# Kernel tuning notes

Hardware: AMD Instinct MI355X
Metric: run time of the kernel (lower is better)

The kernel has to match this reference:

```python
import jax, jax.numpy as jnp
import numpy as np

B, H, W, C = 32, 32, 32, 768
E = 4          # num_experts
TOPK = 2
HD = int(C * 0.25)  # 192, expert hidden dim


def setup_inputs() -> dict:
    key = jax.random.key(0)
    ks = jax.random.split(key, 7)
    x = jax.random.normal(ks[0], (B, H, W, C), dtype=jnp.float32)
    # router: nn.Linear(C, E), weight [E, C] init N(0, 0.02), bias zeros
    router_w = jax.random.normal(ks[1], (E, C), dtype=jnp.float32) * 0.02
    router_b = jnp.zeros((E,), dtype=jnp.float32)
    # per-expert MLP: fc1 [E, HD, C], fc2 [E, C, HD] (torch Linear weight layout)
    fc1_w = jax.random.normal(ks[2], (E, HD, C), dtype=jnp.float32) * (1.0 / np.sqrt(C))
    fc1_b = jax.random.normal(ks[3], (E, HD), dtype=jnp.float32) * 0.01
    fc2_w = jax.random.normal(ks[4], (E, C, HD), dtype=jnp.float32) * (1.0 / np.sqrt(HD))
    fc2_b = jax.random.normal(ks[5], (E, C), dtype=jnp.float32) * 0.01
    return {"x": x, "router_w": router_w, "router_b": router_b,
            "fc1_w": fc1_w, "fc1_b": fc1_b, "fc2_w": fc2_w, "fc2_b": fc2_b}


def reference(x, router_w, router_b, fc1_w, fc1_b, fc2_w, fc2_b):
    b, h, w, c = x.shape
    xt = x.reshape(b, h * w, c)                              # [B, S, C]
    # --- router: softmax + top-k + renormalize ---
    logits = jnp.einsum('bsc,ec->bse', xt, router_w) + router_b
    probs = jax.nn.softmax(logits, axis=-1)                  # [B, S, E]
    topk_w, topk_idx = jax.lax.top_k(probs, TOPK)            # [B, S, K]
    topk_w = topk_w / (jnp.sum(topk_w, axis=-1, keepdims=True) + 1e-8)
    # per-expert combine weight: sum over k of weight where idx==e -> [B, S, E]
    combine = jnp.sum(jax.nn.one_hot(topk_idx, E, dtype=xt.dtype)
                      * topk_w[..., None], axis=-2)          # [B, S, E]
    # --- all experts densely (same math as masked gather/scatter) ---
    # fc1 + exact GELU: [B, S, E, HD]
    hmid = jax.nn.gelu(jnp.einsum('bsc,ehc->bseh', xt, fc1_w) + fc1_b,
                       approximate=False)
    # weight tokens before fc2 to avoid [B,S,E,C] intermediate
    hw = hmid * combine[..., None]                           # [B, S, E, HD]
    out = jnp.einsum('bseh,ech->bsc', hw, fc2_w)
    out = out + jnp.einsum('bse,ec->bsc', combine, fc2_b)    # weighted fc2 bias
    return out.reshape(b, h, w, c)
```

## Files before the change

kernel.cpp:

```cpp
#include <hip/hip_runtime.h>
#include <hip/hip_bf16.h>
#include <math.h>

typedef __attribute__((ext_vector_type(8))) __bf16 bf16x8;
typedef __attribute__((ext_vector_type(4))) float f32x4;
typedef __attribute__((ext_vector_type(4))) unsigned short u16x4;

#define TOKENS 32768
#define CDIM   768
#define SLOTCAP 33536
#define MT_TILES 262
#define RBLOCKS 1024

__device__ __forceinline__ void async_copy16(const void* g, void* l) {
    __builtin_amdgcn_global_load_lds(
        (const __attribute__((address_space(1))) void*)g,
        (__attribute__((address_space(3))) void*)l, 16, 0, 0);
}

__device__ __forceinline__ float fast_gelu(float v) {
    float x  = v * 0.70710678118654752f;
    float ax = fabsf(x);
    float t  = __builtin_amdgcn_rcpf(1.0f + 0.3275911f * ax);
    float poly = t * (0.254829592f +
                 t * (-0.284496736f +
                 t * (1.421413741f +
                 t * (-1.453152027f +
                 t * 1.061405429f))));
    float erfv = 1.0f - poly * __expf(-x * x);
    erfv = copysignf(erfv, x);
    return 0.5f * v * (1.0f + erfv);
}

__device__ __forceinline__ int pair_lo(int p) { return p < 3 ? 0 : (p < 5 ? 1 : 2); }
__device__ __forceinline__ int pair_hi(int p) { return p < 3 ? p + 1 : (p < 5 ? p - 1 : 3); }

__device__ __forceinline__ void bucket_offs(const int* __restrict__ meta, int* offs) {
    int run = 0;
#pragma unroll
    for (int p = 0; p < 6; ++p) {
        offs[p] = run;
        run += ((meta[p] + 127) >> 7) << 7;
    }
}

__global__ __launch_bounds__(256) void prep_weights(
    const float* __restrict__ fc1w, const float* __restrict__ fc2w,
    __hip_bfloat16* __restrict__ b1, __hip_bfloat16* __restrict__ b2t,
    int* __restrict__ slots, float2* __restrict__ swt, int* __restrict__ meta)
{
    int idx = blockIdx.x * 256 + threadIdx.x;
    if (idx < 32) meta[idx] = 0;
    if (idx < SLOTCAP) { slots[idx] = -1; swt[idx] = make_float2(0.f, 0.f); }
    b1[idx] = __float2bfloat16(fc1w[idx]);
    int c = idx / 768;
    int r = idx - c * 768;
    int e = r / 192;
    int h = r - e * 192;
    b2t[idx] = __float2bfloat16(fc2w[((size_t)e * 768 + c) * 192 + h]);
}

__global__ __launch_bounds__(256) void router_convert(
    const float* __restrict__ x, const float* __restrict__ rw,
    const float* __restrict__ rb,
    __hip_bfloat16* __restrict__ xb,
    int* __restrict__ pairid, float2* __restrict__ wpair, int* __restrict__ meta)
{
    __shared__ int rc[6];
    if (threadIdx.x < 6) rc[threadIdx.x] = 0;
    __syncthreads();

    const int wave = threadIdx.x >> 6;
    const int lane = threadIdx.x & 63;
    const int wid  = blockIdx.x * 4 + wave;
    const int el   = lane * 4;

    float4 wv[4][3];
#pragma unroll
    for (int e = 0; e < 4; ++e)
#pragma unroll
        for (int t = 0; t < 3; ++t)
            wv[e][t] = *(const float4*)(rw + e * CDIM + t * 256 + el);
    float rbv[4];
#pragma unroll
    for (int e = 0; e < 4; ++e) rbv[e] = rb[e];

    for (int it = 0; it < 8; ++it) {
        const int token = wid * 8 + it;
        const float* xr = x + (size_t)token * CDIM;

        float4 v[3];
#pragma unroll
        for (int t = 0; t < 3; ++t) v[t] = *(const float4*)(xr + t * 256 + el);

        unsigned short* xrow = (unsigned short*)xb + (size_t)token * CDIM;
#pragma unroll
        for (int t = 0; t < 3; ++t) {
            alignas(8) __hip_bfloat16 hb[4];
            hb[0] = __float2bfloat16(v[t].x);
            hb[1] = __float2bfloat16(v[t].y);
            hb[2] = __float2bfloat16(v[t].z);
            hb[3] = __float2bfloat16(v[t].w);
            *(u16x4*)(xrow + t * 256 + el) = *(const u16x4*)hb;
        }

        float s[4];
#pragma unroll
        for (int e = 0; e < 4; ++e) {
            s[e] = v[0].x * wv[e][0].x + v[0].y * wv[e][0].y
                 + v[0].z * wv[e][0].z + v[0].w * wv[e][0].w
                 + v[1].x * wv[e][1].x + v[1].y * wv[e][1].y
                 + v[1].z * wv[e][1].z + v[1].w * wv[e][1].w
                 + v[2].x * wv[e][2].x + v[2].y * wv[e][2].y
                 + v[2].z * wv[e][2].z + v[2].w * wv[e][2].w;
        }
#pragma unroll
        for (int e = 0; e < 4; ++e) {
            float vv = s[e];
            vv += __shfl_xor(vv, 32); vv += __shfl_xor(vv, 16); vv += __shfl_xor(vv, 8);
            vv += __shfl_xor(vv, 4);  vv += __shfl_xor(vv, 2);  vv += __shfl_xor(vv, 1);
            s[e] = vv;
        }
        float lg[4], p[4];
#pragma unroll
        for (int e = 0; e < 4; ++e) lg[e] = s[e] + rbv[e];
        float mx = fmaxf(fmaxf(lg[0], lg[1]), fmaxf(lg[2], lg[3]));
        float ps = 0.f;
#pragma unroll
        for (int e = 0; e < 4; ++e) { p[e] = __expf(lg[e] - mx); ps += p[e]; }
#pragma unroll
        for (int e = 0; e < 4; ++e) p[e] /= ps;
        int a = 0;
#pragma unroll
        for (int e = 1; e < 4; ++e) if (p[e] > p[a]) a = e;
        int b = (a == 0) ? 1 : 0;
#pragma unroll
        for (int e = 0; e < 4; ++e) if (e != a && p[e] > p[b]) b = e;
        float wsum = p[a] + p[b] + 1e-8f;
        if (lane == 0) {
            int lo = a < b ? a : b;
            int hi = a < b ? b : a;
            int pid = (lo == 0) ? hi - 1 : (lo == 1 ? hi + 1 : 5);
            pairid[token] = pid;
            wpair[token] = make_float2(p[lo] / wsum, p[hi] / wsum);
            atomicAdd(&rc[pid], 1);
        }
    }
    __syncthreads();
    if (threadIdx.x < 6 && rc[threadIdx.x])
        atomicAdd(&meta[threadIdx.x], rc[threadIdx.x]);
}

__global__ __launch_bounds__(256) void scatter_tokens(
    const int* __restrict__ pairid, const float2* __restrict__ wpair,
    int* __restrict__ slots, float2* __restrict__ swt, int* __restrict__ meta)
{
    __shared__ int sc[6], sb[6], soff[6];
    int tid = threadIdx.x;
    if (tid < 6) sc[tid] = 0;
    __syncthreads();
    int t = blockIdx.x * 256 + tid;
    int p = pairid[t];
    int r = atomicAdd(&sc[p], 1);
    __syncthreads();
    if (tid == 0) {
        int offs[6];
        bucket_offs(meta, offs);
#pragma unroll
        for (int q = 0; q < 6; ++q) soff[q] = offs[q];
    }
    if (tid < 6) sb[tid] = sc[tid] ? atomicAdd(&meta[16 + tid], sc[tid]) : 0;
    __syncthreads();
    int pos = soff[p] + sb[p] + r;
    slots[pos] = t;
    swt[pos] = wpair[t];
}

#define BM 128
#define BN 128
#define BK 64

template <int MODE, int K, int NT>
__global__ __launch_bounds__(256) void gemm_moe(
    const __hip_bfloat16* __restrict__ A, const __hip_bfloat16* __restrict__ Bt,
    const int* __restrict__ slots, const float2* __restrict__ swt,
    const int* __restrict__ meta,
    const float* __restrict__ bias1,
    const float* __restrict__ bias2,
    __hip_bfloat16* __restrict__ HW,
    float* __restrict__ OUT)
{
    __shared__ __hip_bfloat16 smem[BM * BK * 4];

    const int tid = threadIdx.x;
    const int wave = tid >> 6, lane = tid & 63;
    const int wm = (wave >> 1) * 64, wn = (wave & 1) * 64;
    const int lrow = lane & 15, quad = lane >> 4;

    constexpr int nwg = MT_TILES * NT;
    constexpr int q = nwg >> 3, rr = nwg & 7;
    const int bid = blockIdx.x;
    const int xcd = bid & 7, sidx = bid >> 3;
    const int wg = (xcd < rr ? xcd * (q + 1) : rr * (q + 1) + (xcd - rr) * q) + sidx;
    const int by = wg / NT;
    const int bx = wg - by * NT;
    const int rowB0 = bx * BN;
    const int rowA0 = by * BM;

    int offs[6];
    bucket_offs(meta, offs);
    int pb = 0;
#pragma unroll
    for (int i = 1; i < 6; ++i) pb += (rowA0 >= offs[i]) ? 1 : 0;
    const int lo = pair_lo(pb), hi = pair_hi(pb);

    const int srow = lane >> 3;
    const int scol = ((lane & 7) ^ srow) * 8;

    size_t aoff[4], boff[4];
    __hip_bfloat16* ldsA[4];
#pragma unroll
    for (int p = 0; p < 4; ++p) {
        int c = wave * 4 + p;
        int arow = c * 8 + srow;
        if (MODE == 0) {
            int tok = slots[rowA0 + arow];
            tok = tok < 0 ? 0 : tok;
            aoff[p] = (size_t)tok * K + scol;
            int grow = rowB0 + arow;
            int gb = (grow < 192) ? lo * 192 + grow : hi * 192 + (grow - 192);
            boff[p] = (size_t)gb * K + scol;
        } else {
            aoff[p] = (size_t)(rowA0 + arow) * K + scol;
            boff[p] = (size_t)(rowB0 + arow) * 768 + scol;
        }
        ldsA[p] = smem + c * 8 * BK;
    }

    auto stage = [&](int buf, int k0) {
        int bo = buf * (2 * BM * BK);
        size_t badd = (MODE == 0) ? (size_t)k0
                    : (size_t)(k0 < 192 ? lo * 192 : hi * 192 - 192) + k0;
#pragma unroll
        for (int p = 0; p < 4; ++p) {
            async_copy16(A + aoff[p] + k0, ldsA[p] + bo);
            async_copy16(Bt + boff[p] + badd, ldsA[p] + bo + BM * BK);
        }
    };

    f32x4 acc[4][4] = {};
    constexpr int NIT = K / BK;

    stage(0, 0);
    __syncthreads();
#pragma unroll
    for (int it = 0; it < NIT; ++it) {
        if (it + 1 < NIT) stage((it + 1) & 1, (it + 1) * BK);
        const __hip_bfloat16* As = smem + (it & 1) * (2 * BM * BK);
        const __hip_bfloat16* Bs = As + BM * BK;
#pragma unroll
        for (int kk = 0; kk < BK; kk += 32) {
            bf16x8 af[4], bfr[4];
#pragma unroll
            for (int i = 0; i < 4; ++i) {
                int row = wm + i * 16 + lrow;
                int gp = ((kk >> 3) + quad) ^ (lrow & 7);
                af[i] = *(const bf16x8*)(&As[row * BK + gp * 8]);
            }
#pragma unroll
            for (int j = 0; j < 4; ++j) {
                int row = wn + j * 16 + lrow;
                int gp = ((kk >> 3) + quad) ^ (lrow & 7);
                bfr[j] = *(const bf16x8*)(&Bs[row * BK + gp * 8]);
            }
#pragma unroll
            for (int i = 0; i < 4; ++i)
#pragma unroll
                for (int j = 0; j < 4; ++j)
                    acc[i][j] = __builtin_amdgcn_mfma_f32_16x16x32_bf16(
                        af[i], bfr[j], acc[i][j], 0, 0, 0);
        }
        __syncthreads();
    }

    if (MODE == 0) {
        const bool hf = (rowB0 + wn) >= 192;
        float b1v[4];
#pragma unroll
        for (int j = 0; j < 4; ++j) {
            int col = rowB0 + wn + j * 16 + lrow;
            int ng = (col < 192) ? lo * 192 + col : hi * 192 + (col - 192);
            b1v[j] = bias1[ng];
        }
#pragma unroll
        for (int i = 0; i < 4; ++i) {
#pragma unroll
            for (int r = 0; r < 4; ++r) {
                int rowl = wm + i * 16 + quad * 4 + r;
                float2 wv = swt[rowA0 + rowl];
                float cwt = hf ? wv.y : wv.x;
                __hip_bfloat16* srow_p = &smem[rowl * BN + wn + lrow];
#pragma unroll
                for (int j = 0; j < 4; ++j) {
                    float v = fast_gelu(acc[i][j][r] + b1v[j]) * cwt;
                    srow_p[j * 16] = __float2bfloat16(v);
                }
            }
        }
        __syncthreads();
#pragma unroll
        for (int t = 0; t < 8; ++t) {
            int idx = t * 256 + tid;
            int row = idx >> 4;
            int c16 = (idx & 15) * 8;
            *(uint4*)(HW + (size_t)(rowA0 + row) * 384 + rowB0 + c16) =
                *(const uint4*)(&smem[row * BN + c16]);
        }
    } else {
        float blo[4], bhi[4];
#pragma unroll
        for (int j = 0; j < 4; ++j) {
            int col = rowB0 + wn + j * 16 + lrow;
            blo[j] = bias2[lo * 768 + col];
            bhi[j] = bias2[hi * 768 + col];
        }
        float* smf = (float*)smem;
#pragma unroll
        for (int i = 0; i < 4; ++i) {
#pragma unroll
            for (int r = 0; r < 4; ++r) {
                int rowl = wm + i * 16 + quad * 4 + r;
                float2 wv = swt[rowA0 + rowl];
                float* sr = smf + rowl * BN + wn + lrow;
#pragma unroll
                for (int j = 0; j < 4; ++j)
                    sr[j * 16] = acc[i][j][r] + wv.x * blo[j] + wv.y * bhi[j];
            }
        }
        __syncthreads();
#pragma unroll
        for (int t = 0; t < 16; ++t) {
            int idx = t * 256 + tid;
            int row = idx >> 5;
            int ch  = idx & 31;
            int tok = slots[rowA0 + row];
            if (tok >= 0)
                *(float4*)(OUT + (size_t)tok * CDIM + rowB0 + ch * 4) =
                    *(const float4*)(smf + row * BN + ch * 4);
        }
    }
}

extern "C" void kernel_launch(void* const* d_in, const int* in_sizes, int n_in,
                              void* d_out, int out_size, void* d_ws, size_t ws_size,
                              hipStream_t stream)
{
    const float* x    = (const float*)d_in[0];
    const float* rw   = (const float*)d_in[1];
    const float* rb   = (const float*)d_in[2];
    const float* fc1w = (const float*)d_in[3];
    const float* fc1b = (const float*)d_in[4];
    const float* fc2w = (const float*)d_in[5];
    const float* fc2b = (const float*)d_in[6];
    float* out = (float*)d_out;

    char* ws = (char*)d_ws;
    __hip_bfloat16* xb   = (__hip_bfloat16*)(ws);
    __hip_bfloat16* hw   = (__hip_bfloat16*)(ws + 50331648);
    __hip_bfloat16* b1   = (__hip_bfloat16*)(ws + 76087296);
    __hip_bfloat16* b2t  = (__hip_bfloat16*)(ws + 77266944);
    float2*         wpr  = (float2*)       (ws + 78446592);
    float2*         swt  = (float2*)       (ws + 78708736);
    int*            pid  = (int*)          (ws + 78977024);
    int*            slots= (int*)          (ws + 79108096);
    int*            meta = (int*)          (ws + 79242240);

    prep_weights<<<2304, 256, 0, stream>>>(fc1w, fc2w, b1, b2t, slots, swt, meta);
    router_convert<<<RBLOCKS, 256, 0, stream>>>(x, rw, rb, xb, pid, wpr, meta);
    scatter_tokens<<<TOKENS / 256, 256, 0, stream>>>(pid, wpr, slots, swt, meta);

    gemm_moe<0, 768, 3><<<MT_TILES * 3, 256, 0, stream>>>(
        xb, b1, slots, swt, meta, fc1b, nullptr, hw, nullptr);
    gemm_moe<1, 384, 6><<<MT_TILES * 6, 256, 0, stream>>>(
        hw, b2t, slots, swt, meta, nullptr, fc2b, nullptr, out);
}
```

Measured before the change: 275.8 us.

## Use full-width 128x384 tile for fc1 so gathered tokens load once

Splits the templated GEMM into dedicated fc1 and fc2 kernels. The fc1 kernel now uses 512 threads and a 128x384 output tile covering both experts' hidden units, so each block loads the gathered token rows once instead of three times across column tiles. It uses 128KB of dynamic shared memory for double-buffered A/B and for the epilogue staging. The cost is a grid of only 262 blocks with very low occupancy, which may underfill the GPU and expose memory latency.

```diff
diff --git a/kernel.cpp b/kernel.cpp
--- a/kernel.cpp
+++ b/kernel.cpp
@@ -176,18 +176,146 @@
     swt[pos] = wpair[t];
 }
 
+__global__ __launch_bounds__(512) void fc1_moe(
+    const __hip_bfloat16* __restrict__ A,
+    const __hip_bfloat16* __restrict__ Bt,
+    const int* __restrict__ slots, const float2* __restrict__ swt,
+    const int* __restrict__ meta, const float* __restrict__ bias1,
+    __hip_bfloat16* __restrict__ HW)
+{
+    extern __shared__ __hip_bfloat16 dynsm[];
+    __hip_bfloat16* Asm = dynsm;
+    __hip_bfloat16* Bsm = dynsm + 2 * 128 * 64;
+
+    const int tid = threadIdx.x;
+    const int wave = tid >> 6, lane = tid & 63;
+    const int wm = (wave >> 2) * 64;
+    const int wn = (wave & 3) * 96;
+    const int lrow = lane & 15, quad = lane >> 4;
+
+    constexpr int nwg = MT_TILES;
+    constexpr int q = nwg >> 3, rr = nwg & 7;
+    const int bid = blockIdx.x;
+    const int xcd = bid & 7, sidx = bid >> 3;
+    const int by = (xcd < rr ? xcd * (q + 1) : rr * (q + 1) + (xcd - rr) * q) + sidx;
+    const int rowA0 = by * 128;
+
+    int offs[6];
+    bucket_offs(meta, offs);
+    int pb = 0;
+#pragma unroll
+    for (int i = 1; i < 6; ++i) pb += (rowA0 >= offs[i]) ? 1 : 0;
+    const int lo = pair_lo(pb), hi = pair_hi(pb);
+
+    const int srow = lane >> 3;
+    const int scol = ((lane & 7) ^ srow) * 8;
+
+    unsigned aoff[2];
+    __hip_bfloat16* ldsA[2];
+#pragma unroll
+    for (int p = 0; p < 2; ++p) {
+        int c = wave * 2 + p;
+        int tok = slots[rowA0 + c * 8 + srow];
+        tok = tok < 0 ? 0 : tok;
+        aoff[p] = (unsigned)tok * 768u + scol;
+        ldsA[p] = Asm + c * 8 * 64;
+    }
+    unsigned boff[6];
+    __hip_bfloat16* ldsB[6];
+#pragma unroll
+    for (int p = 0; p < 6; ++p) {
+        int c = wave * 6 + p;
+        int grow = c * 8 + srow;
+        int gb = (grow < 192) ? lo * 192 + grow : hi * 192 + (grow - 192);
+        boff[p] = (unsigned)gb * 768u + scol;
+        ldsB[p] = Bsm + c * 8 * 64;
+    }
+
+    auto stage = [&](int buf, int k0) {
+#pragma unroll
+        for (int p = 0; p < 2; ++p)
+            async_copy16(A + aoff[p] + k0, ldsA[p] + buf * (128 * 64));
+#pragma unroll
+        for (int p = 0; p < 6; ++p)
+            async_copy16(Bt + boff[p] + k0, ldsB[p] + buf * (384 * 64));
+    };
+
+    f32x4 acc[4][6] = {};
+
+    stage(0, 0);
+    __syncthreads();
+#pragma unroll
+    for (int it = 0; it < 12; ++it) {
+        if (it + 1 < 12) stage((it + 1) & 1, (it + 1) * 64);
+        const __hip_bfloat16* As = Asm + (it & 1) * (128 * 64);
+        const __hip_bfloat16* Bs = Bsm + (it & 1) * (384 * 64);
+#pragma unroll
+        for (int kk = 0; kk < 64; kk += 32) {
+            bf16x8 af[4], bfr[6];
+#pragma unroll
+            for (int i = 0; i < 4; ++i) {
+                int row = wm + i * 16 + lrow;
+                int gp = ((kk >> 3) + quad) ^ (lrow & 7);
+                af[i] = *(const bf16x8*)(&As[row * 64 + gp * 8]);
+            }
+#pragma unroll
+            for (int j = 0; j < 6; ++j) {
+                int row = wn + j * 16 + lrow;
+                int gp = ((kk >> 3) + quad) ^ (lrow & 7);
+                bfr[j] = *(const bf16x8*)(&Bs[row * 64 + gp * 8]);
+            }
+#pragma unroll
+            for (int i = 0; i < 4; ++i)
+#pragma unroll
+                for (int j = 0; j < 6; ++j)
+                    acc[i][j] = __builtin_amdgcn_mfma_f32_16x16x32_bf16(
+                        af[i], bfr[j], acc[i][j], 0, 0, 0);
+        }
+        __syncthreads();
+    }
+
+    float b1v[6];
+#pragma unroll
+    for (int j = 0; j < 6; ++j) {
+        int col = wn + j * 16 + lrow;
+        int ng = (col < 192) ? lo * 192 + col : hi * 192 + (col - 192);
+        b1v[j] = bias1[ng];
+    }
+#pragma unroll
+    for (int i = 0; i < 4; ++i) {
+#pragma unroll
+        for (int r = 0; r < 4; ++r) {
+            int rowl = wm + i * 16 + quad * 4 + r;
+            float2 wv = swt[rowA0 + rowl];
+            __hip_bfloat16* sr = dynsm + rowl * 384 + wn + lrow;
+#pragma unroll
+            for (int j = 0; j < 6; ++j) {
+                float cwt = ((wn + j * 16) >= 192) ? wv.y : wv.x;
+                float v = fast_gelu(acc[i][j][r] + b1v[j]) * cwt;
+                sr[j * 16] = __float2bfloat16(v);
+            }
+        }
+    }
+    __syncthreads();
+#pragma unroll
+    for (int t = 0; t < 12; ++t) {
+        int idx = t * 512 + tid;
+        int row = idx / 48;
+        int c = idx - row * 48;
+        *(uint4*)(HW + (size_t)(rowA0 + row) * 384 + c * 8) =
+            *(const uint4*)(dynsm + row * 384 + c * 8);
+    }
+}
+
 #define BM 128
 #define BN 128
 #define BK 64
 
-template <int MODE, int K, int NT>
-__global__ __launch_bounds__(256) void gemm_moe(
-    const __hip_bfloat16* __restrict__ A, const __hip_bfloat16* __restrict__ Bt,
+__global__ __launch_bounds__(256) void fc2_moe(
+    const __hip_bfloat16* __restrict__ A,
+    const __hip_bfloat16* __restrict__ Bt,
     const int* __restrict__ slots, const float2* __restrict__ swt,
-    const int* __restrict__ meta,
-    const float* __restrict__ bias1,
-    const float* __restrict__ bias2,
-    __hip_bfloat16* __restrict__ HW,
+    const int* __restrict__ meta, const float* __restrict__ bias2,
     float* __restrict__ OUT)
 {
     __shared__ __hip_bfloat16 smem[BM * BK * 4];
@@ -197,6 +325,7 @@
     const int wm = (wave >> 1) * 64, wn = (wave & 1) * 64;
     const int lrow = lane & 15, quad = lane >> 4;
 
+    constexpr int NT = 6;
     constexpr int nwg = MT_TILES * NT;
     constexpr int q = nwg >> 3, rr = nwg & 7;
     const int bid = blockIdx.x;
@@ -223,24 +352,14 @@
     for (int p = 0; p < 4; ++p) {
         int c = wave * 4 + p;
         int arow = c * 8 + srow;
-        if (MODE == 0) {
-            int tok = slots[rowA0 + arow];
-            tok = tok < 0 ? 0 : tok;
-            aoff[p] = (size_t)tok * K + scol;
-            int grow = rowB0 + arow;
-            int gb = (grow < 192) ? lo * 192 + grow : hi * 192 + (grow - 192);
-            boff[p] = (size_t)gb * K + scol;
-        } else {
-            aoff[p] = (size_t)(rowA0 + arow) * K + scol;
-            boff[p] = (size_t)(rowB0 + arow) * 768 + scol;
-        }
+        aoff[p] = (size_t)(rowA0 + arow) * 384 + scol;
+        boff[p] = (size_t)(rowB0 + arow) * 768 + scol;
         ldsA[p] = smem + c * 8 * BK;
     }
 
     auto stage = [&](int buf, int k0) {
         int bo = buf * (2 * BM * BK);
-        size_t badd = (MODE == 0) ? (size_t)k0
-                    : (size_t)(k0 < 192 ? lo * 192 : hi * 192 - 192) + k0;
+        size_t badd = (size_t)(k0 < 192 ? lo * 192 : hi * 192 - 192) + k0;
 #pragma unroll
         for (int p = 0; p < 4; ++p) {
             async_copy16(A + aoff[p] + k0, ldsA[p] + bo);
@@ -249,7 +368,7 @@
     };
 
     f32x4 acc[4][4] = {};
-    constexpr int NIT = K / BK;
+    constexpr int NIT = 384 / BK;
 
     stage(0, 0);
     __syncthreads();
@@ -283,71 +402,36 @@
         __syncthreads();
     }
 
-    if (MODE == 0) {
-        const bool hf = (rowB0 + wn) >= 192;
-        float b1v[4];
-#pragma unroll
-        for (int j = 0; j < 4; ++j) {
-            int col = rowB0 + wn + j * 16 + lrow;
-            int ng = (col < 192) ? lo * 192 + col : hi * 192 + (col - 192);
-            b1v[j] = bias1[ng];
-        }
-#pragma unroll
-        for (int i = 0; i < 4; ++i) {
-#pragma unroll
-            for (int r = 0; r < 4; ++r) {
-                int rowl = wm + i * 16 + quad * 4 + r;
-                float2 wv = swt[rowA0 + rowl];
-                float cwt = hf ? wv.y : wv.x;
-                __hip_bfloat16* srow_p = &smem[rowl * BN + wn + lrow];
-#pragma unroll
-                for (int j = 0; j < 4; ++j) {
-                    float v = fast_gelu(acc[i][j][r] + b1v[j]) * cwt;
-                    srow_p[j * 16] = __float2bfloat16(v);
-                }
-            }
-        }
-        __syncthreads();
-#pragma unroll
-        for (int t = 0; t < 8; ++t) {
-            int idx = t * 256 + tid;
-            int row = idx >> 4;
-            int c16 = (idx & 15) * 8;
-            *(uint4*)(HW + (size_t)(rowA0 + row) * 384 + rowB0 + c16) =
-                *(const uint4*)(&smem[row * BN + c16]);
-        }
-    } else {
-        float blo[4], bhi[4];
-#pragma unroll
-        for (int j = 0; j < 4; ++j) {
-            int col = rowB0 + wn + j * 16 + lrow;
-            blo[j] = bias2[lo * 768 + col];
-            bhi[j] = bias2[hi * 768 + col];
-        }
-        float* smf = (float*)smem;
-#pragma unroll
-        for (int i = 0; i < 4; ++i) {
-#pragma unroll
-            for (int r = 0; r < 4; ++r) {
-                int rowl = wm + i * 16 + quad * 4 + r;
-                float2 wv = swt[rowA0 + rowl];
-                float* sr = smf + rowl * BN + wn + lrow;
-#pragma unroll
-                for (int j = 0; j < 4; ++j)
-                    sr[j * 16] = acc[i][j][r] + wv.x * blo[j] + wv.y * bhi[j];
-            }
-        }
-        __syncthreads();
-#pragma unroll
-        for (int t = 0; t < 16; ++t) {
-            int idx = t * 256 + tid;
-            int row = idx >> 5;
-            int ch  = idx & 31;
-            int tok = slots[rowA0 + row];
-            if (tok >= 0)
-                *(float4*)(OUT + (size_t)tok * CDIM + rowB0 + ch * 4) =
-                    *(const float4*)(smf + row * BN + ch * 4);
-        }
+    float blo[4], bhi[4];
+#pragma unroll
+    for (int j = 0; j < 4; ++j) {
+        int col = rowB0 + wn + j * 16 + lrow;
+        blo[j] = bias2[lo * 768 + col];
+        bhi[j] = bias2[hi * 768 + col];
+    }
+    float* smf = (float*)smem;
+#pragma unroll
+    for (int i = 0; i < 4; ++i) {
+#pragma unroll
+        for (int r = 0; r < 4; ++r) {
+            int rowl = wm + i * 16 + quad * 4 + r;
+            float2 wv = swt[rowA0 + rowl];
+            float* sr = smf + rowl * BN + wn + lrow;
+#pragma unroll
+            for (int j = 0; j < 4; ++j)
+                sr[j * 16] = acc[i][j][r] + wv.x * blo[j] + wv.y * bhi[j];
+        }
+    }
+    __syncthreads();
+#pragma unroll
+    for (int t = 0; t < 16; ++t) {
+        int idx = t * 256 + tid;
+        int row = idx >> 5;
+        int ch  = idx & 31;
+        int tok = slots[rowA0 + row];
+        if (tok >= 0)
+            *(float4*)(OUT + (size_t)tok * CDIM + rowB0 + ch * 4) =
+                *(const float4*)(smf + row * BN + ch * 4);
     }
 }
 
@@ -379,8 +463,8 @@
     router_convert<<<RBLOCKS, 256, 0, stream>>>(x, rw, rb, xb, pid, wpr, meta);
     scatter_tokens<<<TOKENS / 256, 256, 0, stream>>>(pid, wpr, slots, swt, meta);
 
-    gemm_moe<0, 768, 3><<<MT_TILES * 3, 256, 0, stream>>>(
-        xb, b1, slots, swt, meta, fc1b, nullptr, hw, nullptr);
-    gemm_moe<1, 384, 6><<<MT_TILES * 6, 256, 0, stream>>>(
-        hw, b2t, slots, swt, meta, nullptr, fc2b, nullptr, out);
-}
+    fc1_moe<<<MT_TILES, 512, 131072, stream>>>(
+        xb, b1, slots, swt, meta, fc1b, hw);
+    fc2_moe<<<MT_TILES * 6, 256, 0, stream>>>(
+        hw, b2t, slots, swt, meta, fc2b, out);
+}
```

New measurement: 288.9 us. 4.7% more time.

## Double K tile depth and drop LDS double buffering in MoE GEMM

Applied to the files above, without the earlier changes.

Raises the GEMM K tile from 64 to 128 and replaces the two-buffer LDS pipeline with one buffer that is loaded and then synchronised each iteration. This halves the number of K iterations and barriers, and LDS per block stays the same, so occupancy should not change. The cost is that global-to-LDS loads no longer overlap with the MFMA compute, which exposes load latency. Offsets also move to 32-bit, and the MODE 1 expert-boundary handling now works per 16-byte group because a 128-wide K tile can cross the 192 boundary.

```diff
diff --git a/kernel.cpp b/kernel.cpp
--- a/kernel.cpp
+++ b/kernel.cpp
@@ -178,7 +178,7 @@
 
 #define BM 128
 #define BN 128
-#define BK 64
+#define BK 128
 
 template <int MODE, int K, int NT>
 __global__ __launch_bounds__(256) void gemm_moe(
@@ -190,7 +190,7 @@
     __hip_bfloat16* __restrict__ HW,
     float* __restrict__ OUT)
 {
-    __shared__ __hip_bfloat16 smem[BM * BK * 4];
+    __shared__ __hip_bfloat16 smem[BM * BK + BN * BK];
 
     const int tid = threadIdx.x;
     const int wave = tid >> 6, lane = tid & 63;
@@ -214,50 +214,58 @@
     for (int i = 1; i < 6; ++i) pb += (rowA0 >= offs[i]) ? 1 : 0;
     const int lo = pair_lo(pb), hi = pair_hi(pb);
 
-    const int srow = lane >> 3;
-    const int scol = ((lane & 7) ^ srow) * 8;
-
-    size_t aoff[4], boff[4];
-    __hip_bfloat16* ldsA[4];
-#pragma unroll
-    for (int p = 0; p < 4; ++p) {
-        int c = wave * 4 + p;
-        int arow = c * 8 + srow;
+    const int sr4 = lane >> 4;
+    const int pg  = lane & 15;
+
+    unsigned aoff[8], boff[8];
+    __hip_bfloat16* ldsA[8];
+#pragma unroll
+    for (int p = 0; p < 8; ++p) {
+        int c = wave * 8 + p;
+        int rt = c * 4 + sr4;
+        int sg = pg ^ (rt & 7);
+        int sg8 = sg * 8;
         if (MODE == 0) {
-            int tok = slots[rowA0 + arow];
+            int tok = slots[rowA0 + rt];
             tok = tok < 0 ? 0 : tok;
-            aoff[p] = (size_t)tok * K + scol;
-            int grow = rowB0 + arow;
+            aoff[p] = (unsigned)tok * 768u + sg8;
+            int grow = rowB0 + rt;
             int gb = (grow < 192) ? lo * 192 + grow : hi * 192 + (grow - 192);
-            boff[p] = (size_t)gb * K + scol;
+            boff[p] = (unsigned)gb * 768u + sg8;
         } else {
-            aoff[p] = (size_t)(rowA0 + arow) * K + scol;
-            boff[p] = (size_t)(rowB0 + arow) * 768 + scol;
-        }
-        ldsA[p] = smem + c * 8 * BK;
-    }
-
-    auto stage = [&](int buf, int k0) {
-        int bo = buf * (2 * BM * BK);
-        size_t badd = (MODE == 0) ? (size_t)k0
-                    : (size_t)(k0 < 192 ? lo * 192 : hi * 192 - 192) + k0;
-#pragma unroll
-        for (int p = 0; p < 4; ++p) {
-            async_copy16(A + aoff[p] + k0, ldsA[p] + bo);
-            async_copy16(Bt + boff[p] + badd, ldsA[p] + bo + BM * BK);
+            aoff[p] = (unsigned)(rowA0 + rt) * 384u + sg8;
+            boff[p] = (unsigned)(rowB0 + rt) * 768u + sg8;
+        }
+        ldsA[p] = smem + c * 512;
+    }
+
+    auto stage = [&](int k0) {
+#pragma unroll
+        for (int p = 0; p < 8; ++p) {
+            async_copy16(A + aoff[p] + k0, ldsA[p]);
+            unsigned badd;
+            if (MODE == 0) {
+                badd = (unsigned)k0;
+            } else {
+                int c = wave * 8 + p;
+                int rt = c * 4 + sr4;
+                int sg8 = (pg ^ (rt & 7)) * 8;
+                int kabs = k0 + sg8;
+                badd = (unsigned)(k0 + (kabs < 192 ? lo * 192 : hi * 192 - 192));
+            }
+            async_copy16(Bt + boff[p] + badd, ldsA[p] + BM * BK);
         }
     };
 
     f32x4 acc[4][4] = {};
     constexpr int NIT = K / BK;
 
-    stage(0, 0);
-    __syncthreads();
 #pragma unroll
     for (int it = 0; it < NIT; ++it) {
-        if (it + 1 < NIT) stage((it + 1) & 1, (it + 1) * BK);
-        const __hip_bfloat16* As = smem + (it & 1) * (2 * BM * BK);
-        const __hip_bfloat16* Bs = As + BM * BK;
+        stage(it * BK);
+        __syncthreads();
+        const __hip_bfloat16* As = smem;
+        const __hip_bfloat16* Bs = smem + BM * BK;
 #pragma unroll
         for (int kk = 0; kk < BK; kk += 32) {
             bf16x8 af[4], bfr[4];
```

After: 280.1 us. No clear change (+1.6%).
